# Kernel tuning notes

Measured on AMD Instinct MI355X. Metric: run time of the kernel, lower is better.

Reference implementation:

```python
import jax, jax.numpy as jnp
import numpy as np

B, N, D_MODEL, N_HEADS = 4, 2048, 1024, 16
D_K = D_MODEL // N_HEADS  # 64


def setup_inputs() -> dict:
    key = jax.random.key(0)
    ks = jax.random.split(key, 7)
    s = 1.0 / np.sqrt(D_MODEL)
    return {
        "Q": jax.random.normal(ks[0], (B, N, D_MODEL), jnp.float32),
        "K": jax.random.normal(ks[1], (B, N, D_MODEL), jnp.float32),
        "V": jax.random.normal(ks[2], (B, N, D_MODEL), jnp.float32),
        "w_q": jax.random.normal(ks[3], (D_MODEL, D_MODEL), jnp.float32) * s,
        "w_k": jax.random.normal(ks[4], (D_MODEL, D_K), jnp.float32) * s,
        "w_v": jax.random.normal(ks[5], (D_MODEL, D_K), jnp.float32) * s,
        "w_o": jax.random.normal(ks[6], (D_MODEL, D_MODEL), jnp.float32) * s,
    }


def reference(Q, K, V, w_q, w_k, w_v, w_o):
    b, n, _ = Q.shape
    # projections: multi-query -> single shared K/V head of width d_k
    q = (Q @ w_q).reshape(b, n, N_HEADS, D_K)   # [b, n, h, d]
    k = K @ w_k                                  # [b, n, d]
    v = V @ w_v                                  # [b, n, d]
    scale = 1.0 / jnp.sqrt(jnp.asarray(D_K, q.dtype))
    scores = jnp.einsum("bnhd,bmd->bhnm", q, k) * scale  # [b, h, n, n]
    # causal mask: query i attends to keys j <= i (strictly-upper positions masked)
    causal = jnp.triu(jnp.ones((n, n), dtype=bool), k=1)
    scores = jnp.where(causal[None, None], -jnp.inf, scores)
    weights = jax.nn.softmax(scores, axis=-1)
    attn = jnp.einsum("bhnm,bmd->bnhd", weights, v).reshape(b, n, D_MODEL)
    return attn @ w_o
```

## Files before the change

kernel.cpp:

```cpp
#include <hip/hip_runtime.h>

typedef __bf16 bf16;
typedef unsigned int u32;
typedef __bf16 bf16x8 __attribute__((ext_vector_type(8)));
typedef float f32x4 __attribute__((ext_vector_type(4)));
typedef float f32x16 __attribute__((ext_vector_type(16)));

#define DEV __device__ __forceinline__

DEV void gload_lds16(const void* g, void* l) {
  __builtin_amdgcn_global_load_lds((const __attribute__((address_space(1))) void*)g,
                                   (__attribute__((address_space(3))) void*)l,
                                   16, 0, 0);
}

DEV u32 pack2(float a, float b) {
  unsigned short ua = __builtin_bit_cast(unsigned short, (bf16)a);
  unsigned short ub = __builtin_bit_cast(unsigned short, (bf16)b);
  return (u32)ua | ((u32)ub << 16);
}

__global__ void transpose_all(const float* __restrict__ wq, const float* __restrict__ wk,
                              const float* __restrict__ wv, const float* __restrict__ wo,
                              bf16* __restrict__ wqT, bf16* __restrict__ wkvT,
                              bf16* __restrict__ woT, float scale_q) {
  __shared__ float tile[32][33];
  int x = blockIdx.x;
  const float* in;
  bf16* out;
  int C;
  float scale = 1.0f;
  int c0;
  if (x < 32)      { in = wq; out = wqT;             C = 1024; c0 = x * 32; scale = scale_q; }
  else if (x < 34) { in = wk; out = wkvT;            C = 64;   c0 = (x - 32) * 32; }
  else if (x < 36) { in = wv; out = wkvT + 64 * 1024; C = 64;  c0 = (x - 34) * 32; }
  else             { in = wo; out = woT;             C = 1024; c0 = (x - 36) * 32; }
  int r0 = blockIdx.y * 32;
  int tx = threadIdx.x & 31, ty = threadIdx.x >> 5;
  for (int i = ty; i < 32; i += 8) tile[i][tx] = in[(size_t)(r0 + i) * C + c0 + tx];
  __syncthreads();
  for (int i = ty; i < 32; i += 8)
    out[(size_t)(c0 + i) * 1024 + r0 + tx] = (bf16)(tile[tx][i] * scale);
}

template <typename OutT>
__global__ __launch_bounds__(256)
void gemm_bt(const bf16* __restrict__ A, const bf16* __restrict__ Bt,
             OutT* __restrict__ C, int M, int N, int K) {
  __shared__ __align__(16) bf16 As[128 * 32];
  __shared__ __align__(16) bf16 Bs[128 * 32];
  const int tid = threadIdx.x;
  const int wid = tid >> 6, lane = tid & 63;
  const int wr = wid >> 1, wc = wid & 1;
  const int lx = lane & 15, g = lane >> 4;
  const size_t bm = (size_t)blockIdx.x * 128;
  const size_t bn = (size_t)blockIdx.y * 128;
  f32x4 acc[4][4] = {};

  for (int k0 = 0; k0 < K; k0 += 32) {
#pragma unroll
    for (int i = 0; i < 2; ++i) {
      int c = i * 256 + wid * 64 + lane;
      const bf16* gp = A + (bm + (size_t)(c >> 2)) * K + k0 + (c & 3) * 8;
      gload_lds16(gp, (char*)As + (size_t)(i * 256 + wid * 64) * 16);
    }
#pragma unroll
    for (int i = 0; i < 2; ++i) {
      int c = i * 256 + wid * 64 + lane;
      const bf16* gp = Bt + (bn + (size_t)(c >> 2)) * K + k0 + (c & 3) * 8;
      gload_lds16(gp, (char*)Bs + (size_t)(i * 256 + wid * 64) * 16);
    }
    __syncthreads();
    bf16x8 af[4], bfr[4];
#pragma unroll
    for (int m = 0; m < 4; ++m)
      af[m] = *(const bf16x8*)&As[(wr * 64 + m * 16 + lx) * 32 + g * 8];
#pragma unroll
    for (int n = 0; n < 4; ++n)
      bfr[n] = *(const bf16x8*)&Bs[(wc * 64 + n * 16 + lx) * 32 + g * 8];
#pragma unroll
    for (int m = 0; m < 4; ++m)
#pragma unroll
      for (int n = 0; n < 4; ++n)
        acc[m][n] = __builtin_amdgcn_mfma_f32_16x16x32_bf16(af[m], bfr[n], acc[m][n], 0, 0, 0);
    __syncthreads();
  }

#pragma unroll
  for (int m = 0; m < 4; ++m)
#pragma unroll
    for (int n = 0; n < 4; ++n) {
      size_t row = bm + wr * 64 + m * 16 + g * 4;
      size_t col = bn + wc * 64 + n * 16 + lx;
#pragma unroll
      for (int j = 0; j < 4; ++j)
        C[(row + j) * N + col] = (OutT)acc[m][n][j];
    }
}

__global__ __launch_bounds__(256)
void proj_kernel(const float* __restrict__ Qf, const float* __restrict__ Kf,
                 const float* __restrict__ Vf, const bf16* __restrict__ wqT,
                 const bf16* __restrict__ wkvT, bf16* __restrict__ qp,
                 bf16* __restrict__ kp, bf16* __restrict__ vTp) {
  const int bid = blockIdx.x;
  const bool isq = bid < 512;
  const float* Af;
  size_t arow, bm, bn;
  const bf16* Bt = isq ? wqT : wkvT;
  if (isq) {
    bm = (size_t)(bid & 63) * 128;
    arow = bm;
    bn = (size_t)(bid >> 6) * 128;
    Af = Qf;
  } else {
    int kv = bid - 512;
    bm = (size_t)kv * 128;
    bn = 0;
    if (kv < 64) { Af = Kf; arow = bm; } else { Af = Vf; arow = bm - 8192; }
  }

  __shared__ __align__(16) bf16 As[128 * 32];
  __shared__ __align__(16) bf16 Bs[128 * 32];
  const int tid = threadIdx.x;
  const int wid = tid >> 6, lane = tid & 63;
  const int wr = wid >> 1, wc = wid & 1;
  const int lx = lane & 15, g = lane >> 4;
  f32x4 acc[4][4] = {};

  for (int k0 = 0; k0 < 1024; k0 += 32) {
    bf16x8 av[2];
#pragma unroll
    for (int i = 0; i < 2; ++i) {
      int c = i * 256 + tid;
      const float* src = Af + (arow + (size_t)(c >> 2)) * 1024 + k0 + (c & 3) * 8;
      float4 x = *(const float4*)src;
      float4 y = *(const float4*)(src + 4);
      bf16x8 v;
      v[0] = (bf16)x.x; v[1] = (bf16)x.y; v[2] = (bf16)x.z; v[3] = (bf16)x.w;
      v[4] = (bf16)y.x; v[5] = (bf16)y.y; v[6] = (bf16)y.z; v[7] = (bf16)y.w;
      av[i] = v;
    }
#pragma unroll
    for (int i = 0; i < 2; ++i) {
      int c = i * 256 + wid * 64 + lane;
      const bf16* gp = Bt + (bn + (size_t)(c >> 2)) * 1024 + k0 + (c & 3) * 8;
      gload_lds16(gp, (char*)Bs + (size_t)(i * 256 + wid * 64) * 16);
    }
#pragma unroll
    for (int i = 0; i < 2; ++i)
      *(bf16x8*)((char*)As + (size_t)(i * 256 + tid) * 16) = av[i];
    __syncthreads();
    bf16x8 af[4], bfr[4];
#pragma unroll
    for (int m = 0; m < 4; ++m)
      af[m] = *(const bf16x8*)&As[(wr * 64 + m * 16 + lx) * 32 + g * 8];
#pragma unroll
    for (int n = 0; n < 4; ++n)
      bfr[n] = *(const bf16x8*)&Bs[(wc * 64 + n * 16 + lx) * 32 + g * 8];
#pragma unroll
    for (int m = 0; m < 4; ++m)
#pragma unroll
      for (int n = 0; n < 4; ++n)
        acc[m][n] = __builtin_amdgcn_mfma_f32_16x16x32_bf16(af[m], bfr[n], acc[m][n], 0, 0, 0);
    __syncthreads();
  }

#pragma unroll
  for (int m = 0; m < 4; ++m)
#pragma unroll
    for (int n = 0; n < 4; ++n) {
      size_t row = bm + wr * 64 + m * 16 + g * 4;
      size_t col = bn + wc * 64 + n * 16 + lx;
#pragma unroll
      for (int j = 0; j < 4; ++j) {
        float v = acc[m][n][j];
        size_t r = row + j;
        if (isq) {
          qp[r * 1024 + col] = (bf16)v;
        } else if (col < 64) {
          if (r < 8192) kp[r * 64 + col] = (bf16)v;
        } else {
          if (r >= 8192) {
            size_t rr = r - 8192;
            size_t bb = rr >> 11, nn = rr & 2047;
            vTp[bb * 131072 + (nn >> 5) * 2048 + (col - 64) * 32 + (nn & 31)] = (bf16)v;
          }
        }
      }
    }
}

__global__ __launch_bounds__(512, 2)
void attn_kernel(const bf16* __restrict__ q, const bf16* __restrict__ k,
                 const bf16* __restrict__ vt, bf16* __restrict__ o) {
  const int hg = blockIdx.y, b = blockIdx.z;
  const int w = threadIdx.x >> 6, lane = threadIdx.x & 63;
  const int lq = lane & 31, hi = lane >> 5;
  const int hw = w & 3, half = w >> 2;
  const int h = hg * 4 + hw;
  const int pairIdx = blockIdx.x;

  __shared__ __align__(16) char Ks[2][2][8192];
  __shared__ __align__(16) char Vs[2][2][8192];
  __shared__ float bc[8][32];
  __shared__ float mpart[4][32], lpart[4][32];

  const bf16* kb = k + (size_t)b * 2048 * 64;
  const char* vbase = (const char*)vt + (size_t)b * 262144;

  auto stageK = [&](int bi, int kt, int sub) {
    int src = (hw * 64 + lane) ^ ((lane >> 3) & 7);
    gload_lds16((const char*)(kb + (size_t)kt * 2048) + src * 16,
                &Ks[half][bi][sub * 4096 + hw * 1024]);
  };
  auto stageV = [&](int bi, int kt, int sub) {
    int gg = hw * 64 + lane;
    int src = (gg & ~3) | ((gg & 3) ^ ((lane >> 3) & 3));
    gload_lds16(vbase + (size_t)kt * 4096 + src * 16,
                &Vs[half][bi][sub * 4096 + hw * 1024]);
  };

  bf16x8 qf[4];
  auto qkt = [&](int cur, int sub) -> f32x16 {
    bf16x8 kf[4];
#pragma unroll
    for (int i = 0; i < 4; ++i)
      kf[i] = *(const bf16x8*)
          &Ks[half][cur][sub * 4096 + ((lq * 8 + i * 2 + hi) ^ (lq & 7)) * 16];
    f32x16 S = {};
#pragma unroll
    for (int i = 0; i < 4; ++i)
      S = __builtin_amdgcn_mfma_f32_32x32x16_bf16(kf[i], qf[i], S, 0, 0, 0);
    return S;
  };
  auto loadV = [&](int cur, int sub, bf16x8 (&vf)[2][2]) {
#pragma unroll
    for (int d = 0; d < 2; ++d)
#pragma unroll
      for (int ks = 0; ks < 2; ++ks)
        vf[d][ks] = *(const bf16x8*)&Vs[half][cur][sub * 4096 +
                        ((d * 32 + lq) * 4 + ((ks * 2 + hi) ^ ((lq >> 1) & 3))) * 16];
  };
  auto rebuild = [&](const u32 wv[8], bf16x8& o0, bf16x8& o1) {
    u32 sw0 = (u32)__shfl_xor((int)wv[0], 32), sw1 = (u32)__shfl_xor((int)wv[1], 32);
    u32 sw2 = (u32)__shfl_xor((int)wv[2], 32), sw3 = (u32)__shfl_xor((int)wv[3], 32);
    u32 sw4 = (u32)__shfl_xor((int)wv[4], 32), sw5 = (u32)__shfl_xor((int)wv[5], 32);
    u32 sw6 = (u32)__shfl_xor((int)wv[6], 32), sw7 = (u32)__shfl_xor((int)wv[7], 32);
    union { u32 d[4]; bf16x8 v; } f0, f1;
    f0.d[0] = hi ? sw2 : wv[0];
    f0.d[1] = hi ? sw3 : wv[1];
    f0.d[2] = hi ? wv[2] : sw0;
    f0.d[3] = hi ? wv[3] : sw1;
    f1.d[0] = hi ? sw6 : wv[4];
    f1.d[1] = hi ? sw7 : wv[5];
    f1.d[2] = hi ? wv[6] : sw4;
    f1.d[3] = hi ? wv[7] : sw5;
    o0 = f0.v;
    o1 = f1.v;
  };
  auto applyMask = [&](f32x16& S) {
#pragma unroll
    for (int r = 0; r < 16; ++r) {
      int kr = (r & 3) + 8 * (r >> 2) + 4 * hi;
      if (kr > lq) S[r] = -__builtin_inff();
    }
  };
  auto vmax16 = [&](const f32x16& S) -> float {
    float pm = fmaxf(fmaxf(S[0], S[1]), S[2]);
    pm = fmaxf(fmaxf(pm, S[3]), S[4]);
    pm = fmaxf(fmaxf(pm, S[5]), S[6]);
    pm = fmaxf(fmaxf(pm, S[7]), S[8]);
    pm = fmaxf(fmaxf(pm, S[9]), S[10]);
    pm = fmaxf(fmaxf(pm, S[11]), S[12]);
    pm = fmaxf(fmaxf(pm, S[13]), S[14]);
    return fmaxf(pm, S[15]);
  };
  auto expPack = [&](const f32x16& S, float mm, u32 (&wv)[8]) -> float {
    float ls = 0.f;
#pragma unroll
    for (int i = 0; i < 8; ++i) {
      float e0 = __builtin_amdgcn_exp2f(S[2 * i] - mm);
      float e1 = __builtin_amdgcn_exp2f(S[2 * i + 1] - mm);
      ls += e0 + e1;
      wv[i] = pack2(e0, e1);
    }
    return ls;
  };

#pragma unroll 1
  for (int rep = 0; rep < 2; ++rep) {
    const int strip = rep ? pairIdx : 63 - pairIdx;
    const int qb = strip * 32;
    const int nt = strip + 1;
    const int c0 = (nt + 1) >> 1;
    const int myBase = half ? c0 : 0;
    const int myCount = half ? nt - c0 : c0;
    const int R = (c0 + 1) >> 1;

    const bf16* qrow = q + (size_t)(b * 2048 + qb + lq) * 1024 + h * 64 + hi * 8;
#pragma unroll
    for (int i = 0; i < 4; ++i) qf[i] = *(const bf16x8*)(qrow + i * 16);

    f32x16 O0 = {}, O1 = {};
    float m = -__builtin_inff(), l = 0.f;

    __syncthreads();
    if (myCount > 0) { stageK(0, myBase, 0); stageV(0, myBase, 0); }
    if (myCount > 1) { stageK(0, myBase + 1, 1); stageV(0, myBase + 1, 1); }
    __syncthreads();
    int cur = 0;

    for (int r2 = 0; r2 < R; ++r2) {
      const int rem = myCount - 2 * r2;
      if (rem > 2) {
        int tn = myBase + 2 * r2 + 2;
        stageK(cur ^ 1, tn, 0);
        stageV(cur ^ 1, tn, 0);
        if (rem > 3) { stageK(cur ^ 1, tn + 1, 1); stageV(cur ^ 1, tn + 1, 1); }
      }

      if (rem > 0) {
        const bool hasB = rem > 1;
        const int tA = myBase + 2 * r2;

        __builtin_amdgcn_s_setprio(1);
        f32x16 SA = qkt(cur, 0);
        f32x16 SB = {};
        if (hasB) SB = qkt(cur, 1);
        __builtin_amdgcn_s_setprio(0);

        if (tA == nt - 1) applyMask(SA);
        if (hasB && tA + 1 == nt - 1) applyMask(SB);

        float pm = vmax16(SA);
        if (hasB) pm = fmaxf(pm, vmax16(SB));
        pm = fmaxf(pm, __shfl_xor(pm, 32));

        if (!__all(pm <= m + 8.0f)) {
          float mn = fmaxf(m, pm);
          float fac = __builtin_amdgcn_exp2f(m - mn);
          m = mn;
          l *= fac;
          if (hi == 0) bc[w][lq] = fac;
          __threadfence_block();
#pragma unroll
          for (int r = 0; r < 16; ++r) {
            float fr = bc[w][(r & 3) + 8 * (r >> 2) + 4 * hi];
            O0[r] *= fr;
            O1[r] *= fr;
          }
        }

        u32 wA[8], wB[8];
        float ls = expPack(SA, m, wA);
        if (hasB) ls += expPack(SB, m, wB);
        ls += __shfl_xor(ls, 32);
        l += ls;

        bf16x8 f0A, f1A;
        rebuild(wA, f0A, f1A);
        bf16x8 vfA[2][2];
        loadV(cur, 0, vfA);
        bf16x8 f0B, f1B;
        bf16x8 vfB[2][2];
        if (hasB) {
          rebuild(wB, f0B, f1B);
          loadV(cur, 1, vfB);
        }

        __builtin_amdgcn_s_setprio(1);
        O0 = __builtin_amdgcn_mfma_f32_32x32x16_bf16(f0A, vfA[0][0], O0, 0, 0, 0);
        O0 = __builtin_amdgcn_mfma_f32_32x32x16_bf16(f1A, vfA[0][1], O0, 0, 0, 0);
        O1 = __builtin_amdgcn_mfma_f32_32x32x16_bf16(f0A, vfA[1][0], O1, 0, 0, 0);
        O1 = __builtin_amdgcn_mfma_f32_32x32x16_bf16(f1A, vfA[1][1], O1, 0, 0, 0);
        if (hasB) {
          O0 = __builtin_amdgcn_mfma_f32_32x32x16_bf16(f0B, vfB[0][0], O0, 0, 0, 0);
          O0 = __builtin_amdgcn_mfma_f32_32x32x16_bf16(f1B, vfB[0][1], O0, 0, 0, 0);
          O1 = __builtin_amdgcn_mfma_f32_32x32x16_bf16(f0B, vfB[1][0], O1, 0, 0, 0);
          O1 = __builtin_amdgcn_mfma_f32_32x32x16_bf16(f1B, vfB[1][1], O1, 0, 0, 0);
        }
        __builtin_amdgcn_s_setprio(0);
      }

      __syncthreads();
      cur ^= 1;
    }

    float* mO = (float*)&Ks[0][0][0];
    const int L = hi * 32 + lq;
    if (half == 1) {
      if (hi == 0) { mpart[hw][lq] = m; lpart[hw][lq] = l; }
      float* base = mO + (size_t)(hw * 64 + L) * 32;
#pragma unroll
      for (int j = 0; j < 16; ++j) base[j ^ (L & 31)] = O0[j];
#pragma unroll
      for (int j = 0; j < 16; ++j) base[(16 + j) ^ (L & 31)] = O1[j];
    }
    __syncthreads();
    if (half == 0) {
      float m1 = mpart[hw][lq], l1 = lpart[hw][lq];
      float M = fmaxf(m, m1);
      float f0 = __builtin_amdgcn_exp2f(m - M);
      float f1 = __builtin_amdgcn_exp2f(m1 - M);
      float Lt = l * f0 + l1 * f1;
      float inv = 1.0f / Lt;
      if (hi == 0) {
        bc[w][lq] = f0 * inv;
        bc[w + 4][lq] = f1 * inv;
      }
      __threadfence_block();
      const float* base = mO + (size_t)(hw * 64 + L) * 32;
#pragma unroll
      for (int r = 0; r < 16; ++r) {
        int row = (r & 3) + 8 * (r >> 2) + 4 * hi;
        float F0 = bc[w][row], F1 = bc[w + 4][row];
        float v0 = O0[r] * F0 + base[r ^ (L & 31)] * F1;
        float v1 = O1[r] * F0 + base[(16 + r) ^ (L & 31)] * F1;
        size_t gbase = (size_t)(b * 2048 + qb + row) * 1024 + h * 64;
        o[gbase + lq] = (bf16)v0;
        o[gbase + 32 + lq] = (bf16)v1;
      }
    }
  }
}

extern "C" void kernel_launch(void* const* d_in, const int* in_sizes, int n_in,
                              void* d_out, int out_size, void* d_ws, size_t ws_size,
                              hipStream_t stream) {
  const float* Q  = (const float*)d_in[0];
  const float* K  = (const float*)d_in[1];
  const float* V  = (const float*)d_in[2];
  const float* wq = (const float*)d_in[3];
  const float* wk = (const float*)d_in[4];
  const float* wv = (const float*)d_in[5];
  const float* wo = (const float*)d_in[6];
  float* out = (float*)d_out;

  char* ws = (char*)d_ws;
  bf16* qp   = (bf16*)(ws + (48ull << 20));
  bf16* ab   = (bf16*)(ws + (64ull << 20));
  bf16* kp   = (bf16*)(ws + (80ull << 20));
  bf16* vTp  = (bf16*)(ws + (81ull << 20));
  bf16* wqT  = (bf16*)(ws + (82ull << 20));
  bf16* woT  = (bf16*)(ws + (84ull << 20));
  bf16* wkvT = (bf16*)(ws + (86ull << 20));

  const float SCALE = 0.125f * 1.44269504088896340736f;
  transpose_all<<<dim3(68, 32), 256, 0, stream>>>(wq, wk, wv, wo, wqT, wkvT, woT, SCALE);

  proj_kernel<<<640, 256, 0, stream>>>(Q, K, V, wqT, wkvT, qp, kp, vTp);

  attn_kernel<<<dim3(32, 4, 4), 512, 0, stream>>>(qp, kp, vTp, ab);

  gemm_bt<float><<<dim3(64, 8), 256, 0, stream>>>(ab, woT, out, 8192, 1024, 1024);
}
```

Before: 168.2 us.

## Single-buffer V tiles and load them alongside QK^T within each step

V tiles go from double-buffered to single-buffered shared memory. They are now staged at the start of each iteration while QK^T and softmax run, and an extra barrier is added before the PV MFMAs read them. This halves V's LDS footprint, which may allow more occupancy, and overlaps the V load with score computation. The cost is a second __syncthreads per iteration and less lead time for V loads, which can leave the PV stage waiting.

```diff
diff --git a/kernel.cpp b/kernel.cpp
--- a/kernel.cpp
+++ b/kernel.cpp
@@ -202,7 +202,7 @@
   const int pairIdx = blockIdx.x;
 
   __shared__ __align__(16) char Ks[2][2][8192];
-  __shared__ __align__(16) char Vs[2][2][8192];
+  __shared__ __align__(16) char Vs[2][8192];
   __shared__ float bc[8][32];
   __shared__ float mpart[4][32], lpart[4][32];
 
@@ -214,11 +214,10 @@
     gload_lds16((const char*)(kb + (size_t)kt * 2048) + src * 16,
                 &Ks[half][bi][sub * 4096 + hw * 1024]);
   };
-  auto stageV = [&](int bi, int kt, int sub) {
+  auto stageV = [&](int kt, int sub) {
     int gg = hw * 64 + lane;
     int src = (gg & ~3) | ((gg & 3) ^ ((lane >> 3) & 3));
-    gload_lds16(vbase + (size_t)kt * 4096 + src * 16,
-                &Vs[half][bi][sub * 4096 + hw * 1024]);
+    gload_lds16(vbase + (size_t)kt * 4096 + src * 16, &Vs[half][sub * 4096 + hw * 1024]);
   };
 
   bf16x8 qf[4];
@@ -234,12 +233,12 @@
       S = __builtin_amdgcn_mfma_f32_32x32x16_bf16(kf[i], qf[i], S, 0, 0, 0);
     return S;
   };
-  auto loadV = [&](int cur, int sub, bf16x8 (&vf)[2][2]) {
+  auto loadV = [&](int sub, bf16x8 (&vf)[2][2]) {
 #pragma unroll
     for (int d = 0; d < 2; ++d)
 #pragma unroll
       for (int ks = 0; ks < 2; ++ks)
-        vf[d][ks] = *(const bf16x8*)&Vs[half][cur][sub * 4096 +
+        vf[d][ks] = *(const bf16x8*)&Vs[half][sub * 4096 +
                         ((d * 32 + lq) * 4 + ((ks * 2 + hi) ^ ((lq >> 1) & 3))) * 16];
   };
   auto rebuild = [&](const u32 wv[8], bf16x8& o0, bf16x8& o1) {
@@ -306,34 +305,35 @@
     float m = -__builtin_inff(), l = 0.f;
 
     __syncthreads();
-    if (myCount > 0) { stageK(0, myBase, 0); stageV(0, myBase, 0); }
-    if (myCount > 1) { stageK(0, myBase + 1, 1); stageV(0, myBase + 1, 1); }
+    if (myCount > 0) stageK(0, myBase, 0);
+    if (myCount > 1) stageK(0, myBase + 1, 1);
     __syncthreads();
     int cur = 0;
 
     for (int r2 = 0; r2 < R; ++r2) {
       const int rem = myCount - 2 * r2;
+      const int tA = myBase + 2 * r2;
+      const bool hasB = rem > 1;
+
+      if (rem > 0) stageV(tA, 0);
+      if (hasB) stageV(tA + 1, 1);
       if (rem > 2) {
-        int tn = myBase + 2 * r2 + 2;
-        stageK(cur ^ 1, tn, 0);
-        stageV(cur ^ 1, tn, 0);
-        if (rem > 3) { stageK(cur ^ 1, tn + 1, 1); stageV(cur ^ 1, tn + 1, 1); }
-      }
-
+        stageK(cur ^ 1, tA + 2, 0);
+        if (rem > 3) stageK(cur ^ 1, tA + 3, 1);
+      }
+
+      f32x16 SA = {}, SB = {};
+      float pm = -__builtin_inff();
       if (rem > 0) {
-        const bool hasB = rem > 1;
-        const int tA = myBase + 2 * r2;
-
         __builtin_amdgcn_s_setprio(1);
-        f32x16 SA = qkt(cur, 0);
-        f32x16 SB = {};
+        SA = qkt(cur, 0);
         if (hasB) SB = qkt(cur, 1);
         __builtin_amdgcn_s_setprio(0);
 
         if (tA == nt - 1) applyMask(SA);
         if (hasB && tA + 1 == nt - 1) applyMask(SB);
 
-        float pm = vmax16(SA);
+        pm = vmax16(SA);
         if (hasB) pm = fmaxf(pm, vmax16(SB));
         pm = fmaxf(pm, __shfl_xor(pm, 32));
 
@@ -351,23 +351,26 @@
             O1[r] *= fr;
           }
         }
-
-        u32 wA[8], wB[8];
+      }
+
+      u32 wA[8], wB[8];
+      bf16x8 f0A, f1A, f0B, f1B;
+      if (rem > 0) {
         float ls = expPack(SA, m, wA);
         if (hasB) ls += expPack(SB, m, wB);
         ls += __shfl_xor(ls, 32);
         l += ls;
-
-        bf16x8 f0A, f1A;
         rebuild(wA, f0A, f1A);
+        if (hasB) rebuild(wB, f0B, f1B);
+      }
+
+      __syncthreads();
+
+      if (rem > 0) {
         bf16x8 vfA[2][2];
-        loadV(cur, 0, vfA);
-        bf16x8 f0B, f1B;
+        loadV(0, vfA);
         bf16x8 vfB[2][2];
-        if (hasB) {
-          rebuild(wB, f0B, f1B);
-          loadV(cur, 1, vfB);
-        }
+        if (hasB) loadV(1, vfB);
 
         __builtin_amdgcn_s_setprio(1);
         O0 = __builtin_amdgcn_mfma_f32_32x32x16_bf16(f0A, vfA[0][0], O0, 0, 0, 0);
```

Result: no change. 166.1 us (-1.3%).
